# Kernel optimization log

Hardware: AMD Instinct MI355X
Metric: run time of the kernel (lower is better)

Reference implementation:

```python
import jax, jax.numpy as jnp
import numpy as np

B, IN, H = 4096, 1024, 1024


def setup_inputs() -> dict:
    key = jax.random.key(0)
    ks = jax.random.split(key, 16)
    u = lambda k, shape: jax.random.uniform(k, shape, jnp.float32, -0.1, 0.1)
    return {
        "x": jax.random.normal(ks[0], (B, IN), jnp.float32),
        "h_prev": jax.random.normal(ks[1], (B, H), jnp.float32),
        "c_prev": jax.random.normal(ks[2], (B, H), jnp.float32),
        "W_ii": u(ks[3], (H, IN)), "W_hi": u(ks[4], (H, H)), "b_i": u(ks[5], (H,)),
        "W_if": u(ks[6], (H, IN)), "W_hf": u(ks[7], (H, H)), "b_f": u(ks[8], (H,)),
        "W_ig": u(ks[9], (H, IN)), "W_hg": u(ks[10], (H, H)), "b_g": u(ks[11], (H,)),
        "W_io": u(ks[12], (H, IN)), "W_ho": u(ks[13], (H, H)), "b_o": u(ks[14], (H,)),
    }


def reference(x, h_prev, c_prev, W_ii, W_hi, b_i, W_if, W_hf, b_f,
              W_ig, W_hg, b_g, W_io, W_ho, b_o):
    # Fuse the 8 gate GEMMs into 2 concatenated-weight GEMMs: [B,IN]@[IN,4H] and [B,H]@[H,4H]
    W_x = jnp.concatenate([W_ii, W_if, W_ig, W_io], axis=0)  # [4H, IN]
    W_h = jnp.concatenate([W_hi, W_hf, W_hg, W_ho], axis=0)  # [4H, H]
    b = jnp.concatenate([b_i, b_f, b_g, b_o])                # [4H]
    gates = x @ W_x.T + h_prev @ W_h.T + b                   # [B, 4H]
    i_t, f_t, g_t, o_t = jnp.split(gates, 4, axis=-1)
    i_t = jax.nn.sigmoid(i_t)
    f_t = jax.nn.sigmoid(f_t)
    g_t = jnp.tanh(g_t)
    o_t = jax.nn.sigmoid(o_t)
    c_t = f_t * c_prev + i_t * g_t
    h_t = o_t * jnp.tanh(c_t)
    return (h_t, (h_t, c_t))
```

## Files before the change

kernel.cpp:

```cpp
#include <hip/hip_runtime.h>
#include <hip/hip_bf16.h>
#include <stdint.h>

#define B_DIM 4096
#define IN_DIM 1024
#define H_DIM 1024
#define K_DIM 2048
#define N_DIM 4096
#define BH (B_DIM * H_DIM)
#define NT 32

typedef __bf16 bf16x8 __attribute__((ext_vector_type(8)));
typedef float  f32x4  __attribute__((ext_vector_type(4)));

__device__ __forceinline__ unsigned short f2b(float f) {
  uint32_t u = __builtin_bit_cast(uint32_t, f);
  u += 0x7fffu + ((u >> 16) & 1u);
  return (unsigned short)(u >> 16);
}

__device__ __forceinline__ void load_lds16(const void* g, void* l) {
  __builtin_amdgcn_global_load_lds(
      (const __attribute__((address_space(1))) uint32_t*)g,
      (__attribute__((address_space(3))) uint32_t*)l, 16, 0, 0);
}

__device__ __forceinline__ void bar() {
  asm volatile("" ::: "memory");
  __builtin_amdgcn_s_barrier();
  asm volatile("" ::: "memory");
}

__device__ __forceinline__ float sigmoidf_(float x) {
  return 1.0f / (1.0f + __expf(-x));
}
__device__ __forceinline__ float tanhf_(float x) {
  float e = __expf(-2.0f * x);
  return (1.0f - e) / (1.0f + e);
}

__global__ void pack_a(const float* __restrict__ x, const float* __restrict__ h,
                       unsigned short* __restrict__ A) {
  int t = blockIdx.x * 256 + threadIdx.x;
  int e = t * 4;
  int b = e >> 11;
  int k = e & 2047;
  const float* src = (k < IN_DIM) ? (x + (size_t)b * IN_DIM + k)
                                  : (h + (size_t)b * H_DIM + (k - IN_DIM));
  f32x4 v = *(const f32x4*)src;
  ushort4 o;
  o.x = f2b(v[0]); o.y = f2b(v[1]); o.z = f2b(v[2]); o.w = f2b(v[3]);
  *(ushort4*)(A + (size_t)b * K_DIM + k) = o;
}

__global__ void pack_w(const float* __restrict__ Wii, const float* __restrict__ Wif,
                       const float* __restrict__ Wig, const float* __restrict__ Wio,
                       const float* __restrict__ Whi, const float* __restrict__ Whf,
                       const float* __restrict__ Whg, const float* __restrict__ Who,
                       unsigned short* __restrict__ W) {
  int t = blockIdx.x * 256 + threadIdx.x;
  int e = t * 4;
  int n = e >> 11;
  int k = e & 2047;
  int gate = n >> 10;
  int j = n & 1023;
  const float* Wx = (gate == 0) ? Wii : (gate == 1) ? Wif : (gate == 2) ? Wig : Wio;
  const float* Wh = (gate == 0) ? Whi : (gate == 1) ? Whf : (gate == 2) ? Whg : Who;
  const float* src = (k < IN_DIM) ? (Wx + (size_t)j * IN_DIM + k)
                                  : (Wh + (size_t)j * H_DIM + (k - IN_DIM));
  f32x4 v = *(const f32x4*)src;
  ushort4 o;
  o.x = f2b(v[0]); o.y = f2b(v[1]); o.z = f2b(v[2]); o.w = f2b(v[3]);
  *(ushort4*)(W + (size_t)n * K_DIM + k) = o;
}


#define STAGE(ldsbase, gbase, kelem) do {                                        \
  const unsigned short* g0_ = (gbase) + (size_t)srow0 * K_DIM + (kelem) + schunk * 8; \
  load_lds16(g0_, (ldsbase) + tid * 8);                                          \
  load_lds16(g0_ + (size_t)64 * K_DIM, (ldsbase) + 4096 + tid * 8);              \
} while (0)

#define PHASE(SLOT, MQ, NQ, STAGE_STMT, VM_WAIT) do {                            \
  const unsigned short* As_ = &lds[SLOT][0][MQ][0];                              \
  const unsigned short* Bs_ = &lds[SLOT][1][NQ][0];                              \
  bf16x8 af[4][2], bq[2][2];                                                     \
  _Pragma("unroll")                                                              \
  for (int m = 0; m < 4; ++m) {                                                  \
    int ro = (wr * 64 + m * 16 + lrow) * 64;                                     \
    af[m][0] = *(const bf16x8*)(As_ + ro + ks0);                                 \
    af[m][1] = *(const bf16x8*)(As_ + ro + ks1);                                 \
  }                                                                              \
  _Pragma("unroll")                                                              \
  for (int n = 0; n < 2; ++n) {                                                  \
    int ro = (wc * 32 + n * 16 + lrow) * 64;                                     \
    bq[n][0] = *(const bf16x8*)(Bs_ + ro + ks0);                                 \
    bq[n][1] = *(const bf16x8*)(Bs_ + ro + ks1);                                 \
  }                                                                              \
  STAGE_STMT;                                                                    \
  bar();                                                                         \
  asm volatile("s_waitcnt lgkmcnt(0)" ::: "memory");                             \
  __builtin_amdgcn_sched_barrier(0);                                             \
  __builtin_amdgcn_s_setprio(1);                                                 \
  _Pragma("unroll")                                                              \
  for (int m = 0; m < 4; ++m)                                                    \
    _Pragma("unroll")                                                            \
    for (int n = 0; n < 2; ++n) {                                                \
      acc[MQ][NQ][m][n] = __builtin_amdgcn_mfma_f32_16x16x32_bf16(               \
          af[m][0], bq[n][0], acc[MQ][NQ][m][n], 0, 0, 0);                       \
      acc[MQ][NQ][m][n] = __builtin_amdgcn_mfma_f32_16x16x32_bf16(               \
          af[m][1], bq[n][1], acc[MQ][NQ][m][n], 0, 0, 0);                       \
    }                                                                            \
  __builtin_amdgcn_s_setprio(0);                                                 \
  __builtin_amdgcn_sched_barrier(0);                                             \
  VM_WAIT;                                                                       \
  bar();                                                                         \
} while (0)

__global__ __launch_bounds__(512, 2) void gemm_gates(
    const unsigned short* __restrict__ A,
    const unsigned short* __restrict__ W,
    float* __restrict__ C) {
  __shared__ unsigned short lds[2][2][2][128 * 64];

  const int tid  = threadIdx.x;
  const int lane = tid & 63;
  const int wid  = tid >> 6;
  const int wr   = wid >> 2;
  const int wc   = wid & 3;
  const int lrow = lane & 15;

  const int b0 = blockIdx.x;
  const int w  = (b0 & 7) * 32 + (b0 >> 3);
  const int bx = w & 15;
  const int by = w >> 4;

  const unsigned short* Ag = A + (size_t)by * 256 * K_DIM;
  const unsigned short* Wg = W + (size_t)bx * 256 * K_DIM;

  const int srow0  = tid >> 3;
  const int schunk = (tid & 7) ^ (srow0 & 7);
  const int ks0 = (((lane >> 4) * 8)) ^ ((lane & 7) << 3);
  const int ks1 = ks0 ^ 32;

  f32x4 acc[2][2][4][2];
#pragma unroll
  for (int a = 0; a < 2; ++a)
#pragma unroll
    for (int b = 0; b < 2; ++b)
#pragma unroll
      for (int m = 0; m < 4; ++m)
#pragma unroll
        for (int n = 0; n < 2; ++n) acc[a][b][m][n] = (f32x4){0.f, 0.f, 0.f, 0.f};

  STAGE(&lds[0][0][0][0], Ag, 0);
  STAGE(&lds[0][1][0][0], Wg, 0);
  STAGE(&lds[0][0][1][0], Ag + 128 * K_DIM, 0);
  STAGE(&lds[0][1][1][0], Wg + 128 * K_DIM, 0);
  STAGE(&lds[1][0][0][0], Ag, 64);
  STAGE(&lds[1][1][0][0], Wg, 64);
  asm volatile("s_waitcnt vmcnt(4)" ::: "memory");
  bar();

  for (int t2 = 0; t2 < NT; t2 += 2) {
    {
      const int t = t2;
      const int k1 = (t + 1) * 64, k2 = (t + 2) * 64;
      PHASE(0, 0, 0, if (t < NT - 1) STAGE(&lds[1][0][1][0], Ag + 128 * K_DIM, k1), );
      PHASE(0, 0, 1, if (t < NT - 1) STAGE(&lds[1][1][1][0], Wg + 128 * K_DIM, k1), );
      PHASE(0, 1, 0, if (t < NT - 2) STAGE(&lds[0][0][0][0], Ag, k2), );
      PHASE(0, 1, 1, if (t < NT - 2) STAGE(&lds[0][1][0][0], Wg, k2),
            asm volatile("s_waitcnt vmcnt(4)" ::: "memory"));
    }
    {
      const int t = t2 + 1;
      const int k1 = (t + 1) * 64, k2 = (t + 2) * 64;
      PHASE(1, 0, 0, if (t < NT - 1) STAGE(&lds[0][0][1][0], Ag + 128 * K_DIM, k1), );
      PHASE(1, 0, 1, if (t < NT - 1) STAGE(&lds[0][1][1][0], Wg + 128 * K_DIM, k1), );
      PHASE(1, 1, 0, if (t < NT - 2) STAGE(&lds[1][0][0][0], Ag, k2), );
      PHASE(1, 1, 1, if (t < NT - 2) STAGE(&lds[1][1][0][0], Wg, k2),
            asm volatile("s_waitcnt vmcnt(4)" ::: "memory"));
    }
  }

  const int rbase = by * 256 + wr * 64 + (lane >> 4) * 4;
  const int cbase = bx * 256 + wc * 32 + lrow;
#pragma unroll
  for (int mq = 0; mq < 2; ++mq)
#pragma unroll
    for (int nq = 0; nq < 2; ++nq)
#pragma unroll
      for (int m = 0; m < 4; ++m)
#pragma unroll
        for (int n = 0; n < 2; ++n) {
          const int row = rbase + mq * 128 + m * 16;
          const int col = cbase + nq * 128 + n * 16;
#pragma unroll
          for (int r = 0; r < 4; ++r)
            C[(size_t)(row + r) * N_DIM + col] = acc[mq][nq][m][n][r];
        }
}

__global__ void lstm_epilogue(const float* __restrict__ gates,
                              const float* __restrict__ c_prev,
                              const float* __restrict__ b_i, const float* __restrict__ b_f,
                              const float* __restrict__ b_g, const float* __restrict__ b_o,
                              float* __restrict__ out) {
  int t = blockIdx.x * 256 + threadIdx.x;
  int e = t * 4;
  int b = e >> 10;
  int j = e & 1023;
  size_t rowbase = (size_t)b * N_DIM;
  f32x4 ig = *(const f32x4*)&gates[rowbase + j];
  f32x4 fg = *(const f32x4*)&gates[rowbase + 1024 + j];
  f32x4 gg = *(const f32x4*)&gates[rowbase + 2048 + j];
  f32x4 og = *(const f32x4*)&gates[rowbase + 3072 + j];
  f32x4 bi = *(const f32x4*)&b_i[j];
  f32x4 bf = *(const f32x4*)&b_f[j];
  f32x4 bg = *(const f32x4*)&b_g[j];
  f32x4 bo = *(const f32x4*)&b_o[j];
  f32x4 cp = *(const f32x4*)&c_prev[e];

  f32x4 h4, c4;
#pragma unroll
  for (int r = 0; r < 4; ++r) {
    float i_t = sigmoidf_(ig[r] + bi[r]);
    float f_t = sigmoidf_(fg[r] + bf[r]);
    float g_t = tanhf_(gg[r] + bg[r]);
    float o_t = sigmoidf_(og[r] + bo[r]);
    float c_t = f_t * cp[r] + i_t * g_t;
    c4[r] = c_t;
    h4[r] = o_t * tanhf_(c_t);
  }
  *(f32x4*)&out[e]          = h4;
  *(f32x4*)&out[BH + e]     = h4;
  *(f32x4*)&out[2 * BH + e] = c4;
}

extern "C" void kernel_launch(void* const* d_in, const int* in_sizes, int n_in,
                              void* d_out, int out_size, void* d_ws, size_t ws_size,
                              hipStream_t stream) {
  const float* x   = (const float*)d_in[0];
  const float* hp  = (const float*)d_in[1];
  const float* cp  = (const float*)d_in[2];
  const float* Wii = (const float*)d_in[3];
  const float* Whi = (const float*)d_in[4];
  const float* bi  = (const float*)d_in[5];
  const float* Wif = (const float*)d_in[6];
  const float* Whf = (const float*)d_in[7];
  const float* bf  = (const float*)d_in[8];
  const float* Wig = (const float*)d_in[9];
  const float* Whg = (const float*)d_in[10];
  const float* bg  = (const float*)d_in[11];
  const float* Wio = (const float*)d_in[12];
  const float* Who = (const float*)d_in[13];
  const float* bo  = (const float*)d_in[14];

  unsigned short* Abf   = (unsigned short*)d_ws;
  unsigned short* Wbf   = (unsigned short*)((char*)d_ws + (16u << 20));
  float*          gates = (float*)((char*)d_ws + (32u << 20));
  float*          out   = (float*)d_out;

  pack_a<<<8192, 256, 0, stream>>>(x, hp, Abf);
  pack_w<<<8192, 256, 0, stream>>>(Wii, Wif, Wig, Wio, Whi, Whf, Whg, Who, Wbf);
  gemm_gates<<<256, 512, 0, stream>>>(Abf, Wbf, gates);
  lstm_epilogue<<<4096, 256, 0, stream>>>(gates, cp, bi, bf, bg, bo, out);
}
```

Baseline: 241.5 us.

## Fuse LSTM epilogue into GEMM via gate-interleaved weight packing; merge pack kernels

Weights are packed so that each 256-column GEMM tile holds matching i/f/g/o columns for 64 hidden units. This lets the gate nonlinearities and the cell update run directly on the accumulators, removing the fp32 gates round-trip through global memory and the separate epilogue kernel. The two pack kernels are merged into one launch. The K loop's staging order and wait counts are reworked, with a peeled tail, to keep more loads in flight. The epilogue stores are strided scalar writes, which may coalesce less well than the old vectorized epilogue.

```diff
diff --git a/kernel.cpp b/kernel.cpp
--- a/kernel.cpp
+++ b/kernel.cpp
@@ -6,7 +6,6 @@
 #define IN_DIM 1024
 #define H_DIM 1024
 #define K_DIM 2048
-#define N_DIM 4096
 #define BH (B_DIM * H_DIM)
 #define NT 32
 
@@ -39,41 +38,48 @@
   return (1.0f - e) / (1.0f + e);
 }
 
-__global__ void pack_a(const float* __restrict__ x, const float* __restrict__ h,
-                       unsigned short* __restrict__ A) {
-  int t = blockIdx.x * 256 + threadIdx.x;
-  int e = t * 4;
-  int b = e >> 11;
-  int k = e & 2047;
-  const float* src = (k < IN_DIM) ? (x + (size_t)b * IN_DIM + k)
-                                  : (h + (size_t)b * H_DIM + (k - IN_DIM));
-  f32x4 v = *(const f32x4*)src;
-  ushort4 o;
-  o.x = f2b(v[0]); o.y = f2b(v[1]); o.z = f2b(v[2]); o.w = f2b(v[3]);
-  *(ushort4*)(A + (size_t)b * K_DIM + k) = o;
-}
-
-__global__ void pack_w(const float* __restrict__ Wii, const float* __restrict__ Wif,
-                       const float* __restrict__ Wig, const float* __restrict__ Wio,
-                       const float* __restrict__ Whi, const float* __restrict__ Whf,
-                       const float* __restrict__ Whg, const float* __restrict__ Who,
-                       unsigned short* __restrict__ W) {
-  int t = blockIdx.x * 256 + threadIdx.x;
-  int e = t * 4;
-  int n = e >> 11;
-  int k = e & 2047;
-  int gate = n >> 10;
-  int j = n & 1023;
-  const float* Wx = (gate == 0) ? Wii : (gate == 1) ? Wif : (gate == 2) ? Wig : Wio;
-  const float* Wh = (gate == 0) ? Whi : (gate == 1) ? Whf : (gate == 2) ? Whg : Who;
-  const float* src = (k < IN_DIM) ? (Wx + (size_t)j * IN_DIM + k)
-                                  : (Wh + (size_t)j * H_DIM + (k - IN_DIM));
-  f32x4 v = *(const f32x4*)src;
-  ushort4 o;
-  o.x = f2b(v[0]); o.y = f2b(v[1]); o.z = f2b(v[2]); o.w = f2b(v[3]);
-  *(ushort4*)(W + (size_t)n * K_DIM + k) = o;
-}
-
+__global__ void pack_all(const float* __restrict__ x, const float* __restrict__ h,
+                         const float* __restrict__ Wii, const float* __restrict__ Wif,
+                         const float* __restrict__ Wig, const float* __restrict__ Wio,
+                         const float* __restrict__ Whi, const float* __restrict__ Whf,
+                         const float* __restrict__ Whg, const float* __restrict__ Who,
+                         unsigned short* __restrict__ A, unsigned short* __restrict__ Wp) {
+  const int bid = blockIdx.x;
+  if (bid < 8192) {
+    int t = bid * 256 + threadIdx.x;
+    int e = t * 4;
+    int b = e >> 11;
+    int k = e & 2047;
+    const float* src = (k < IN_DIM) ? (x + (size_t)b * IN_DIM + k)
+                                    : (h + (size_t)b * H_DIM + (k - IN_DIM));
+    f32x4 v = *(const f32x4*)src;
+    ushort4 o;
+    o.x = f2b(v[0]); o.y = f2b(v[1]); o.z = f2b(v[2]); o.w = f2b(v[3]);
+    *(ushort4*)(A + (size_t)b * K_DIM + k) = o;
+  } else {
+    int t = (bid - 8192) * 256 + threadIdx.x;
+    int e = t * 4;
+    int n = e >> 11;
+    int k = e & 2047;
+    int r = n & 255;
+    int gate = ((r >> 7) << 1) | ((r >> 4) & 1);
+    int j = ((n >> 8) << 6) + (((r >> 5) & 3) << 4) + (r & 15);
+    const float* Wx = (gate == 0) ? Wii : (gate == 1) ? Wif : (gate == 2) ? Wig : Wio;
+    const float* Wh = (gate == 0) ? Whi : (gate == 1) ? Whf : (gate == 2) ? Whg : Who;
+    const float* src = (k < IN_DIM) ? (Wx + (size_t)j * IN_DIM + k)
+                                    : (Wh + (size_t)j * H_DIM + (k - IN_DIM));
+    f32x4 v = *(const f32x4*)src;
+    ushort4 o;
+    o.x = f2b(v[0]); o.y = f2b(v[1]); o.z = f2b(v[2]); o.w = f2b(v[3]);
+    *(ushort4*)(Wp + (size_t)n * K_DIM + k) = o;
+  }
+}
+
+
+#define VM8 asm volatile("s_waitcnt vmcnt(8)" ::: "memory")
+#define VM4 asm volatile("s_waitcnt vmcnt(4)" ::: "memory")
+#define VM2 asm volatile("s_waitcnt vmcnt(2)" ::: "memory")
+#define VM0 asm volatile("s_waitcnt vmcnt(0)" ::: "memory")
 
 #define STAGE(ldsbase, gbase, kelem) do {                                        \
   const unsigned short* g0_ = (gbase) + (size_t)srow0 * K_DIM + (kelem) + schunk * 8; \
@@ -117,10 +123,13 @@
   bar();                                                                         \
 } while (0)
 
-__global__ __launch_bounds__(512, 2) void gemm_gates(
+__global__ __launch_bounds__(512, 2) void gemm_lstm(
     const unsigned short* __restrict__ A,
-    const unsigned short* __restrict__ W,
-    float* __restrict__ C) {
+    const unsigned short* __restrict__ Wp,
+    const float* __restrict__ c_prev,
+    const float* __restrict__ b_i, const float* __restrict__ b_f,
+    const float* __restrict__ b_g, const float* __restrict__ b_o,
+    float* __restrict__ out) {
   __shared__ unsigned short lds[2][2][2][128 * 64];
 
   const int tid  = threadIdx.x;
@@ -135,12 +144,12 @@
   const int bx = w & 15;
   const int by = w >> 4;
 
-  const unsigned short* Ag = A + (size_t)by * 256 * K_DIM;
-  const unsigned short* Wg = W + (size_t)bx * 256 * K_DIM;
+  const unsigned short* Ag = A  + (size_t)by * 256 * K_DIM;
+  const unsigned short* Wg = Wp + (size_t)bx * 256 * K_DIM;
 
   const int srow0  = tid >> 3;
   const int schunk = (tid & 7) ^ (srow0 & 7);
-  const int ks0 = (((lane >> 4) * 8)) ^ ((lane & 7) << 3);
+  const int ks0 = ((lane >> 4) * 8) ^ ((lane & 7) << 3);
   const int ks1 = ks0 ^ 32;
 
   f32x4 acc[2][2][4][2];
@@ -159,82 +168,58 @@
   STAGE(&lds[0][1][1][0], Wg + 128 * K_DIM, 0);
   STAGE(&lds[1][0][0][0], Ag, 64);
   STAGE(&lds[1][1][0][0], Wg, 64);
-  asm volatile("s_waitcnt vmcnt(4)" ::: "memory");
+  VM4;
   bar();
 
-  for (int t2 = 0; t2 < NT; t2 += 2) {
+  for (int t2 = 0; t2 < NT - 2; t2 += 2) {
     {
-      const int t = t2;
-      const int k1 = (t + 1) * 64, k2 = (t + 2) * 64;
-      PHASE(0, 0, 0, if (t < NT - 1) STAGE(&lds[1][0][1][0], Ag + 128 * K_DIM, k1), );
-      PHASE(0, 0, 1, if (t < NT - 1) STAGE(&lds[1][1][1][0], Wg + 128 * K_DIM, k1), );
-      PHASE(0, 1, 0, if (t < NT - 2) STAGE(&lds[0][0][0][0], Ag, k2), );
-      PHASE(0, 1, 1, if (t < NT - 2) STAGE(&lds[0][1][0][0], Wg, k2),
-            asm volatile("s_waitcnt vmcnt(4)" ::: "memory"));
+      const int k1 = (t2 + 1) * 64, k2 = (t2 + 2) * 64;
+      PHASE(0, 0, 0, STAGE(&lds[1][1][1][0], Wg + 128 * K_DIM, k1), VM8);
+      PHASE(0, 0, 1, STAGE(&lds[1][0][1][0], Ag + 128 * K_DIM, k1), VM8);
+      PHASE(0, 1, 0, STAGE(&lds[0][0][0][0], Ag, k2), );
+      PHASE(0, 1, 1, STAGE(&lds[0][1][0][0], Wg, k2), VM8);
     }
     {
-      const int t = t2 + 1;
-      const int k1 = (t + 1) * 64, k2 = (t + 2) * 64;
-      PHASE(1, 0, 0, if (t < NT - 1) STAGE(&lds[0][0][1][0], Ag + 128 * K_DIM, k1), );
-      PHASE(1, 0, 1, if (t < NT - 1) STAGE(&lds[0][1][1][0], Wg + 128 * K_DIM, k1), );
-      PHASE(1, 1, 0, if (t < NT - 2) STAGE(&lds[1][0][0][0], Ag, k2), );
-      PHASE(1, 1, 1, if (t < NT - 2) STAGE(&lds[1][1][0][0], Wg, k2),
-            asm volatile("s_waitcnt vmcnt(4)" ::: "memory"));
+      const int k1 = (t2 + 2) * 64, k2 = (t2 + 3) * 64;
+      PHASE(1, 0, 0, STAGE(&lds[0][1][1][0], Wg + 128 * K_DIM, k1), VM8);
+      PHASE(1, 0, 1, STAGE(&lds[0][0][1][0], Ag + 128 * K_DIM, k1), VM8);
+      PHASE(1, 1, 0, STAGE(&lds[1][0][0][0], Ag, k2), );
+      PHASE(1, 1, 1, STAGE(&lds[1][1][0][0], Wg, k2), VM8);
     }
   }
-
-  const int rbase = by * 256 + wr * 64 + (lane >> 4) * 4;
-  const int cbase = bx * 256 + wc * 32 + lrow;
+  {
+    const int k1 = (NT - 1) * 64;
+    PHASE(0, 0, 0, STAGE(&lds[1][1][1][0], Wg + 128 * K_DIM, k1), VM8);
+    PHASE(0, 0, 1, STAGE(&lds[1][0][1][0], Ag + 128 * K_DIM, k1), VM8);
+    PHASE(0, 1, 0, , );
+    PHASE(0, 1, 1, , VM4);
+    PHASE(1, 0, 0, , VM2);
+    PHASE(1, 0, 1, , VM0);
+    PHASE(1, 1, 0, , );
+    PHASE(1, 1, 1, , );
+  }
+
+  const int j  = bx * 64 + wc * 16 + lrow;
+  const float biv = b_i[j], bfv = b_f[j], bgv = b_g[j], bov = b_o[j];
+  const int rb = by * 256 + wr * 64 + (lane >> 4) * 4;
 #pragma unroll
   for (int mq = 0; mq < 2; ++mq)
 #pragma unroll
-    for (int nq = 0; nq < 2; ++nq)
-#pragma unroll
-      for (int m = 0; m < 4; ++m)
-#pragma unroll
-        for (int n = 0; n < 2; ++n) {
-          const int row = rbase + mq * 128 + m * 16;
-          const int col = cbase + nq * 128 + n * 16;
-#pragma unroll
-          for (int r = 0; r < 4; ++r)
-            C[(size_t)(row + r) * N_DIM + col] = acc[mq][nq][m][n][r];
-        }
-}
-
-__global__ void lstm_epilogue(const float* __restrict__ gates,
-                              const float* __restrict__ c_prev,
-                              const float* __restrict__ b_i, const float* __restrict__ b_f,
-                              const float* __restrict__ b_g, const float* __restrict__ b_o,
-                              float* __restrict__ out) {
-  int t = blockIdx.x * 256 + threadIdx.x;
-  int e = t * 4;
-  int b = e >> 10;
-  int j = e & 1023;
-  size_t rowbase = (size_t)b * N_DIM;
-  f32x4 ig = *(const f32x4*)&gates[rowbase + j];
-  f32x4 fg = *(const f32x4*)&gates[rowbase + 1024 + j];
-  f32x4 gg = *(const f32x4*)&gates[rowbase + 2048 + j];
-  f32x4 og = *(const f32x4*)&gates[rowbase + 3072 + j];
-  f32x4 bi = *(const f32x4*)&b_i[j];
-  f32x4 bf = *(const f32x4*)&b_f[j];
-  f32x4 bg = *(const f32x4*)&b_g[j];
-  f32x4 bo = *(const f32x4*)&b_o[j];
-  f32x4 cp = *(const f32x4*)&c_prev[e];
-
-  f32x4 h4, c4;
-#pragma unroll
-  for (int r = 0; r < 4; ++r) {
-    float i_t = sigmoidf_(ig[r] + bi[r]);
-    float f_t = sigmoidf_(fg[r] + bf[r]);
-    float g_t = tanhf_(gg[r] + bg[r]);
-    float o_t = sigmoidf_(og[r] + bo[r]);
-    float c_t = f_t * cp[r] + i_t * g_t;
-    c4[r] = c_t;
-    h4[r] = o_t * tanhf_(c_t);
-  }
-  *(f32x4*)&out[e]          = h4;
-  *(f32x4*)&out[BH + e]     = h4;
-  *(f32x4*)&out[2 * BH + e] = c4;
+    for (int m = 0; m < 4; ++m)
+#pragma unroll
+      for (int r = 0; r < 4; ++r) {
+        const int row = rb + mq * 128 + m * 16 + r;
+        const float iv = sigmoidf_(acc[mq][0][m][0][r] + biv);
+        const float fv = sigmoidf_(acc[mq][0][m][1][r] + bfv);
+        const float gv = tanhf_(acc[mq][1][m][0][r] + bgv);
+        const float ov = sigmoidf_(acc[mq][1][m][1][r] + bov);
+        const size_t idx = (size_t)row * H_DIM + j;
+        const float cv = fv * c_prev[idx] + iv * gv;
+        const float hv = ov * tanhf_(cv);
+        out[idx]          = hv;
+        out[BH + idx]     = hv;
+        out[2 * BH + idx] = cv;
+      }
 }
 
 extern "C" void kernel_launch(void* const* d_in, const int* in_sizes, int n_in,
@@ -256,13 +241,11 @@
   const float* Who = (const float*)d_in[13];
   const float* bo  = (const float*)d_in[14];
 
-  unsigned short* Abf   = (unsigned short*)d_ws;
-  unsigned short* Wbf   = (unsigned short*)((char*)d_ws + (16u << 20));
-  float*          gates = (float*)((char*)d_ws + (32u << 20));
-  float*          out   = (float*)d_out;
-
-  pack_a<<<8192, 256, 0, stream>>>(x, hp, Abf);
-  pack_w<<<8192, 256, 0, stream>>>(Wii, Wif, Wig, Wio, Whi, Whf, Whg, Who, Wbf);
-  gemm_gates<<<256, 512, 0, stream>>>(Abf, Wbf, gates);
-  lstm_epilogue<<<4096, 256, 0, stream>>>(gates, cp, bi, bf, bg, bo, out);
-}
+  unsigned short* Abf = (unsigned short*)d_ws;
+  unsigned short* Wbf = (unsigned short*)((char*)d_ws + (16u << 20));
+  float*          out = (float*)d_out;
+
+  pack_all<<<16384, 256, 0, stream>>>(x, hp, Wii, Wif, Wig, Wio,
+                                      Whi, Whf, Whg, Who, Abf, Wbf);
+  gemm_lstm<<<256, 512, 0, stream>>>(Abf, Wbf, cp, bi, bf, bg, bo, out);
+}
```

After: 214.9 us. 11.0% less time.
